# Optimization experiments

Measured on AMD Instinct MI355X. Metric: run time of the kernel, lower is better.

Reference implementation:

```python
import jax, jax.numpy as jnp
import numpy as np

N = 100000      # nodes
E = 1600000     # edges (avg degree 16)
F_IN, F_HID, F_OUT = 128, 64, 47


def setup_inputs() -> dict:
    key = jax.random.key(0)
    k1, k2, k3, k4 = jax.random.split(key, 4)
    x = jax.random.normal(k1, (N, F_IN), jnp.float32)
    edge_index = jax.random.randint(k2, (2, E), 0, N, jnp.int32)
    W1 = jax.random.normal(k3, (F_IN, F_HID), jnp.float32) * (1.0 / np.sqrt(F_IN))
    b1 = jnp.zeros((F_HID,), jnp.float32)
    W2 = jax.random.normal(k4, (F_HID, F_OUT), jnp.float32) * (1.0 / np.sqrt(F_HID))
    b2 = jnp.zeros((F_OUT,), jnp.float32)
    return {"x": x, "edge_index": edge_index, "W1": W1, "b1": b1, "W2": W2, "b2": b2}


def _gcn_conv(x, W, b, src, dst, n):
    """GCNConv with self-loops and symmetric normalization:
       out = D^{-1/2} (A + I) D^{-1/2} X W + b
    """
    xw = x @ W                                   # [N, F_out] transform first (small GEMM)
    # degree of A + I computed over destination nodes
    deg = jnp.ones((n,), xw.dtype).at[dst].add(1.0)      # [N]
    dinv = jax.lax.rsqrt(deg)                            # deg^{-1/2}
    norm = dinv[src] * dinv[dst]                         # [E]
    msg = xw[src] * norm[:, None]                        # [E, F_out] gather
    agg = jnp.zeros_like(xw).at[dst].add(msg)            # scatter-add aggregate
    agg = agg + xw * (1.0 / deg)[:, None]                # self-loop term: norm = 1/deg
    return agg + b


def reference(x, edge_index, W1, b1, W2, b2):
    src, dst = edge_index[0], edge_index[1]
    n = x.shape[0]
    h = _gcn_conv(x, W1, b1, src, dst, n)
    h = jax.nn.relu(h)
    # dropout is identity in eval mode (deterministic baseline)
    h = _gcn_conv(h, W2, b2, src, dst, n)
    return jax.nn.log_softmax(h, axis=1)
```

## Files before the change

### kernel.cpp

```cpp
#include <hip/hip_runtime.h>
#include <hip/hip_bf16.h>
#include <math.h>


#define CAP 48
#define NBSHIFT 8
#define SCNODES 256
#define BCAP 6144
typedef unsigned short u16;

__device__ __forceinline__ u16 f2bf(float f) {
    __hip_bfloat16 h = __float2bfloat16(f);
    return *reinterpret_cast<u16*>(&h);
}
__device__ __forceinline__ float bf2f(u16 u) {
    return __uint_as_float(((unsigned)u) << 16);
}


#define KC 32
#define KCP 36
#define GEMM_SMEM (64 * KCP * 4 + KC * 64 * 4)

__global__ __launch_bounds__(256) void gemm1_bin(const float* __restrict__ X,
                                                 const float* __restrict__ W,
                                                 u16* __restrict__ OUT,
                                                 const int* __restrict__ src,
                                                 const int* __restrict__ dst,
                                                 int* __restrict__ gtail,
                                                 int2* __restrict__ bucketed,
                                                 int N, int E, int NB, int seg, int GB) {
    __shared__ __align__(16) char smem[GEMM_SMEM];
    const int t = threadIdx.x;

    if ((int)blockIdx.x < GB) {
        float* xs = (float*)smem;
        float* Wp = (float*)(smem + 64 * KCP * 4);
        const int row0 = blockIdx.x * 64;
        const int c4 = (t & 15) * 4;
        const int r4 = (t >> 4) * 4;
        float acc[4][4] = {};

        for (int k0 = 0; k0 < 128; k0 += KC) {
            const float4* W4 = reinterpret_cast<const float4*>(W + k0 * 64);
            #pragma unroll
            for (int i = t; i < KC * 16; i += 256)
                reinterpret_cast<float4*>(Wp)[i] = W4[i];
            #pragma unroll
            for (int i = t; i < 64 * 8; i += 256) {
                int r = i >> 3, kq = i & 7;
                int m = row0 + r;
                float4 v = make_float4(0.f, 0.f, 0.f, 0.f);
                if (m < N) v = *reinterpret_cast<const float4*>(&X[(size_t)m * 128 + k0 + kq * 4]);
                *reinterpret_cast<float4*>(&xs[r * KCP + kq * 4]) = v;
            }
            __syncthreads();

            for (int k = 0; k < KC; k += 4) {
                float4 A[4], B[4];
                #pragma unroll
                for (int i = 0; i < 4; i++)
                    A[i] = *reinterpret_cast<const float4*>(&xs[(r4 + i) * KCP + k]);
                #pragma unroll
                for (int kk = 0; kk < 4; kk++)
                    B[kk] = *reinterpret_cast<const float4*>(&Wp[(k + kk) * 64 + c4]);
                const float* Af = reinterpret_cast<const float*>(A);
                const float* Bf = reinterpret_cast<const float*>(B);
                #pragma unroll
                for (int i = 0; i < 4; i++)
                    #pragma unroll
                    for (int kk = 0; kk < 4; kk++) {
                        float av = Af[i * 4 + kk];
                        #pragma unroll
                        for (int j = 0; j < 4; j++)
                            acc[i][j] = fmaf(av, Bf[kk * 4 + j], acc[i][j]);
                    }
            }
            __syncthreads();
        }
        #pragma unroll
        for (int i = 0; i < 4; i++) {
            int m = row0 + r4 + i;
            if (m >= N) continue;
            ushort4 o;
            o.x = f2bf(acc[i][0]); o.y = f2bf(acc[i][1]);
            o.z = f2bf(acc[i][2]); o.w = f2bf(acc[i][3]);
            *reinterpret_cast<ushort4*>(&OUT[(size_t)m * 64 + c4]) = o;
        }
    } else {
        int* hist = (int*)smem;
        int* base = hist + 512;
        const int bid = blockIdx.x - GB;

        const int b0 = bid * seg;
        const int b1 = min(b0 + seg, E);
        for (int i = t; i < NB; i += 256) hist[i] = 0;
        __syncthreads();
        for (int e = b0 + t; e < b1; e += 256)
            atomicAdd(&hist[dst[e] >> NBSHIFT], 1);
        __syncthreads();
        for (int i = t; i < NB; i += 256) {
            int h = hist[i];
            base[i] = h ? atomicAdd(&gtail[i], h) : 0;
            hist[i] = 0;
        }
        __syncthreads();
        for (int e = b0 + t; e < b1; e += 256) {
            int d = dst[e];
            int b = d >> NBSHIFT;
            int idx = base[b] + atomicAdd(&hist[b], 1);
            if (idx < BCAP) bucketed[(size_t)b * BCAP + idx] = make_int2(src[e], d);
        }
    }
}


__global__ __launch_bounds__(512) void scatter_csr(const int2* __restrict__ bucketed,
                                                   const int* __restrict__ gtail,
                                                   int* __restrict__ cnt,
                                                   int* __restrict__ csr_src,
                                                   float* __restrict__ dinv, int N) {
    __shared__ int cntL[SCNODES];
    __shared__ __align__(16) int csrL[SCNODES * CAP];
    const int b = blockIdx.x;
    const int t = threadIdx.x;
    for (int i = t; i < SCNODES; i += 512) cntL[i] = 0;
    __syncthreads();

    int n = gtail[b]; if (n > BCAP) n = BCAP;
    const int2* p = bucketed + (size_t)b * BCAP;
    for (int i = t; i < n; i += 512) {
        int2 e = p[i];
        int l = e.y & (SCNODES - 1);
        int slot = atomicAdd(&cntL[l], 1);
        if (slot < CAP) csrL[l * CAP + slot] = e.x;
    }
    __syncthreads();

    const int v0 = b << NBSHIFT;
    const int lim = min(SCNODES, N - v0);
    if (lim <= 0) return;
    int4* dst4 = reinterpret_cast<int4*>(&csr_src[(size_t)v0 * CAP]);
    const int4* src4 = reinterpret_cast<const int4*>(csrL);
    for (int i = t; i < lim * (CAP / 4); i += 512) dst4[i] = src4[i];
    for (int i = t; i < lim; i += 512) {
        int cv = cntL[i];
        cnt[v0 + i] = cv;
        dinv[v0 + i] = rsqrtf((float)cv + 1.0f);
    }
}


__global__ __launch_bounds__(256) void gemm2_tiled(const u16* __restrict__ X,
                                                   const float* __restrict__ W,
                                                   u16* __restrict__ OUT, int N) {
    __shared__ __align__(16) char smem[GEMM_SMEM];
    float* xs = (float*)smem;
    float* Wp = (float*)(smem + 64 * KCP * 4);
    const int t = threadIdx.x;
    const int row0 = blockIdx.x * 64;
    const int c4 = (t & 15) * 4;
    const int r4 = (t >> 4) * 4;
    float acc[4][4] = {};

    for (int k0 = 0; k0 < 64; k0 += KC) {
        for (int i = t; i < KC * 64; i += 256) {
            int k = i >> 6, c = i & 63;
            Wp[i] = (c < 47) ? W[(k0 + k) * 47 + c] : 0.f;
        }
        {
            int i = t;
            int r = i >> 2, kq = i & 3;
            int m = row0 + r;
            uint4 q = make_uint4(0u, 0u, 0u, 0u);
            if (m < N) q = *reinterpret_cast<const uint4*>(&X[(size_t)m * 64 + k0 + kq * 8]);
            float f0o = bf2f(q.x & 0xffffu), f1 = bf2f(q.x >> 16);
            float f2 = bf2f(q.y & 0xffffu), f3 = bf2f(q.y >> 16);
            float f4 = bf2f(q.z & 0xffffu), f5 = bf2f(q.z >> 16);
            float f6 = bf2f(q.w & 0xffffu), f7 = bf2f(q.w >> 16);
            float* dstp = &xs[r * KCP + kq * 8];
            *reinterpret_cast<float4*>(dstp)     = make_float4(f0o, f1, f2, f3);
            *reinterpret_cast<float4*>(dstp + 4) = make_float4(f4, f5, f6, f7);
        }
        __syncthreads();

        for (int k = 0; k < KC; k += 4) {
            float4 A[4], B[4];
            #pragma unroll
            for (int i = 0; i < 4; i++)
                A[i] = *reinterpret_cast<const float4*>(&xs[(r4 + i) * KCP + k]);
            #pragma unroll
            for (int kk = 0; kk < 4; kk++)
                B[kk] = *reinterpret_cast<const float4*>(&Wp[(k + kk) * 64 + c4]);
            const float* Af = reinterpret_cast<const float*>(A);
            const float* Bf = reinterpret_cast<const float*>(B);
            #pragma unroll
            for (int i = 0; i < 4; i++)
                #pragma unroll
                for (int kk = 0; kk < 4; kk++) {
                    float av = Af[i * 4 + kk];
                    #pragma unroll
                    for (int j = 0; j < 4; j++)
                        acc[i][j] = fmaf(av, Bf[kk * 4 + j], acc[i][j]);
                }
        }
        __syncthreads();
    }
    #pragma unroll
    for (int i = 0; i < 4; i++) {
        int m = row0 + r4 + i;
        if (m >= N) continue;
        ushort4 o;
        o.x = f2bf(acc[i][0]); o.y = f2bf(acc[i][1]);
        o.z = f2bf(acc[i][2]); o.w = f2bf(acc[i][3]);
        *reinterpret_cast<ushort4*>(&OUT[(size_t)m * 64 + c4]) = o;
    }
}

__device__ __forceinline__ void fma_bf8(uint4 q, float w, float* acc) {
    acc[0] = fmaf(__uint_as_float(q.x << 16),          w, acc[0]);
    acc[1] = fmaf(__uint_as_float(q.x & 0xffff0000u),  w, acc[1]);
    acc[2] = fmaf(__uint_as_float(q.y << 16),          w, acc[2]);
    acc[3] = fmaf(__uint_as_float(q.y & 0xffff0000u),  w, acc[3]);
    acc[4] = fmaf(__uint_as_float(q.z << 16),          w, acc[4]);
    acc[5] = fmaf(__uint_as_float(q.z & 0xffff0000u),  w, acc[5]);
    acc[6] = fmaf(__uint_as_float(q.w << 16),          w, acc[6]);
    acc[7] = fmaf(__uint_as_float(q.w & 0xffff0000u),  w, acc[7]);
}


__global__ __launch_bounds__(256, 4) void agg1_relu(const u16* __restrict__ xw,
                                                    const int* __restrict__ csr_src,
                                                    const int* __restrict__ cnt,
                                                    const float* __restrict__ dinv,
                                                    const float* __restrict__ bias,
                                                    u16* __restrict__ h, int N) {
    const int wid = (blockIdx.x * 256 + threadIdx.x) >> 6;
    const int lane = threadIdx.x & 63;
    const int v = wid * 2 + (lane >> 5);
    if (wid * 2 >= N) return;
    const bool okv = v < N;
    const int vs = okv ? v : 0;
    const int hl = lane & 31;
    int c = okv ? cnt[vs] : 0; if (c > CAP - 1) c = CAP - 1;
    const float dv = okv ? dinv[vs] : 0.f;
    int rawA = csr_src[vs * CAP + hl];
    int sA; float wA;
    if (hl < c)        { sA = rawA; wA = dinv[sA] * dv; }
    else if (hl == c)  { sA = vs;   wA = dv * dv; }
    else               { sA = 0;    wA = 0.f; }

    int ce = c + 1;
    int cemax = max(ce, __shfl_xor(ce, 32));
    const int r = hl >> 3, b = hl & 7;
    const int base = lane & 32;
    float acc[8] = {};

    {
        int s8[8]; float w8[8];
        #pragma unroll
        for (int u = 0; u < 8; u++) {
            int e = u * 4 + r;
            s8[u] = __shfl(sA, base + e);
            w8[u] = __shfl(wA, base + e);
        }
        uint4 q8[8];
        #pragma unroll
        for (int u = 0; u < 8; u++)
            if (u * 4 < cemax)
                q8[u] = *reinterpret_cast<const uint4*>(&xw[(size_t)s8[u] * 64 + b * 8]);
        #pragma unroll
        for (int u = 0; u < 8; u++)
            if (u * 4 < cemax) fma_bf8(q8[u], w8[u], acc);
    }
    if (cemax > 32) {
        int rawB = csr_src[vs * CAP + 32 + hl];
        int hl32 = hl + 32;
        int sB; float wB;
        if (hl32 < c)       { sB = rawB; wB = dinv[sB] * dv; }
        else if (hl32 == c) { sB = vs;   wB = dv * dv; }
        else                { sB = 0;    wB = 0.f; }
        int s8[8]; float w8[8];
        #pragma unroll
        for (int u = 0; u < 8; u++) {
            int e = u * 4 + r;
            s8[u] = __shfl(sB, base + e);
            w8[u] = __shfl(wB, base + e);
        }
        uint4 q8[8];
        #pragma unroll
        for (int u = 0; u < 8; u++)
            if (32 + u * 4 < cemax)
                q8[u] = *reinterpret_cast<const uint4*>(&xw[(size_t)s8[u] * 64 + b * 8]);
        #pragma unroll
        for (int u = 0; u < 8; u++)
            if (32 + u * 4 < cemax) fma_bf8(q8[u], w8[u], acc);
    }

    #pragma unroll
    for (int u = 0; u < 8; u++) {
        acc[u] += __shfl_xor(acc[u], 8);
        acc[u] += __shfl_xor(acc[u], 16);
    }
    if (r == 0 && okv) {
        ushort4 oA, oB;
        oA.x = f2bf(fmaxf(acc[0] + bias[b * 8 + 0], 0.f));
        oA.y = f2bf(fmaxf(acc[1] + bias[b * 8 + 1], 0.f));
        oA.z = f2bf(fmaxf(acc[2] + bias[b * 8 + 2], 0.f));
        oA.w = f2bf(fmaxf(acc[3] + bias[b * 8 + 3], 0.f));
        oB.x = f2bf(fmaxf(acc[4] + bias[b * 8 + 4], 0.f));
        oB.y = f2bf(fmaxf(acc[5] + bias[b * 8 + 5], 0.f));
        oB.z = f2bf(fmaxf(acc[6] + bias[b * 8 + 6], 0.f));
        oB.w = f2bf(fmaxf(acc[7] + bias[b * 8 + 7], 0.f));
        u16* dstp = &h[(size_t)v * 64 + b * 8];
        *reinterpret_cast<ushort4*>(dstp)     = oA;
        *reinterpret_cast<ushort4*>(dstp + 4) = oB;
    }
}


__global__ __launch_bounds__(256, 4) void agg2_lsm(const u16* __restrict__ hw,
                                                   const int* __restrict__ csr_src,
                                                   const int* __restrict__ cnt,
                                                   const float* __restrict__ dinv,
                                                   const float* __restrict__ bias,
                                                   float* __restrict__ out, int N) {
    const int wid = (blockIdx.x * 256 + threadIdx.x) >> 6;
    const int lane = threadIdx.x & 63;
    const int v = wid * 2 + (lane >> 5);
    if (wid * 2 >= N) return;
    const bool okv = v < N;
    const int vs = okv ? v : 0;
    const int hl = lane & 31;
    int c = okv ? cnt[vs] : 0; if (c > CAP - 1) c = CAP - 1;
    const float dv = okv ? dinv[vs] : 0.f;
    int rawA = csr_src[vs * CAP + hl];
    int sA; float wA;
    if (hl < c)        { sA = rawA; wA = dinv[sA] * dv; }
    else if (hl == c)  { sA = vs;   wA = dv * dv; }
    else               { sA = 0;    wA = 0.f; }

    int ce = c + 1;
    int cemax = max(ce, __shfl_xor(ce, 32));
    const int r = hl >> 3, b = hl & 7;
    const int base = lane & 32;
    float acc[8] = {};

    {
        int s8[8]; float w8[8];
        #pragma unroll
        for (int u = 0; u < 8; u++) {
            int e = u * 4 + r;
            s8[u] = __shfl(sA, base + e);
            w8[u] = __shfl(wA, base + e);
        }
        uint4 q8[8];
        #pragma unroll
        for (int u = 0; u < 8; u++)
            if (u * 4 < cemax)
                q8[u] = *reinterpret_cast<const uint4*>(&hw[(size_t)s8[u] * 64 + b * 8]);
        #pragma unroll
        for (int u = 0; u < 8; u++)
            if (u * 4 < cemax) fma_bf8(q8[u], w8[u], acc);
    }
    if (cemax > 32) {
        int rawB = csr_src[vs * CAP + 32 + hl];
        int hl32 = hl + 32;
        int sB; float wB;
        if (hl32 < c)       { sB = rawB; wB = dinv[sB] * dv; }
        else if (hl32 == c) { sB = vs;   wB = dv * dv; }
        else                { sB = 0;    wB = 0.f; }
        int s8[8]; float w8[8];
        #pragma unroll
        for (int u = 0; u < 8; u++) {
            int e = u * 4 + r;
            s8[u] = __shfl(sB, base + e);
            w8[u] = __shfl(wB, base + e);
        }
        uint4 q8[8];
        #pragma unroll
        for (int u = 0; u < 8; u++)
            if (32 + u * 4 < cemax)
                q8[u] = *reinterpret_cast<const uint4*>(&hw[(size_t)s8[u] * 64 + b * 8]);
        #pragma unroll
        for (int u = 0; u < 8; u++)
            if (32 + u * 4 < cemax) fma_bf8(q8[u], w8[u], acc);
    }

    #pragma unroll
    for (int u = 0; u < 8; u++) {
        acc[u] += __shfl_xor(acc[u], 8);
        acc[u] += __shfl_xor(acc[u], 16);
    }
    const int f0 = b * 8;
    float val[8];
    #pragma unroll
    for (int u = 0; u < 8; u++) {
        int f = f0 + u;
        val[u] = (f < 47) ? acc[u] + bias[f] : -INFINITY;
    }
    float m = val[0];
    #pragma unroll
    for (int u = 1; u < 8; u++) m = fmaxf(m, val[u]);
    m = fmaxf(m, __shfl_xor(m, 1));
    m = fmaxf(m, __shfl_xor(m, 2));
    m = fmaxf(m, __shfl_xor(m, 4));
    float s = 0.f;
    #pragma unroll
    for (int u = 0; u < 8; u++)
        s += (f0 + u < 47) ? __expf(val[u] - m) : 0.f;
    s += __shfl_xor(s, 1);
    s += __shfl_xor(s, 2);
    s += __shfl_xor(s, 4);
    float ls = m + __logf(s);
    if (r == 0 && okv) {
        #pragma unroll
        for (int u = 0; u < 8; u++) {
            int f = f0 + u;
            if (f < 47) out[(size_t)v * 47 + f] = val[u] - ls;
        }
    }
}


extern "C" void kernel_launch(void* const* d_in, const int* in_sizes, int n_in,
                              void* d_out, int out_size, void* d_ws, size_t ws_size,
                              hipStream_t stream) {
    const float* x  = (const float*)d_in[0];
    const int*   ei = (const int*)d_in[1];
    const float* W1 = (const float*)d_in[2];
    const float* b1 = (const float*)d_in[3];
    const float* W2 = (const float*)d_in[4];
    const float* b2 = (const float*)d_in[5];
    float* out = (float*)d_out;

    const int N = in_sizes[0] / 128;
    const int E = in_sizes[1] / 2;
    const int* src = ei;
    const int* dst = ei + E;
    const int NB = ((N - 1) >> NBSHIFT) + 1;

    char* ws = (char*)d_ws;
    size_t off = 0;
    auto alloc = [&](size_t bytes) {
        void* p = ws + off;
        off += (bytes + 255) & ~(size_t)255;
        return p;
    };
    int*   cnt      = (int*)  alloc((size_t)N * 4);
    int*   gtail    = (int*)  alloc((size_t)512 * 4);
    float* dinv     = (float*)alloc((size_t)N * 4);
    int*   csr_src  = (int*)  alloc(((size_t)N * CAP + 64) * 4);
    u16*   xw1      = (u16*)  alloc((size_t)N * 64 * 2);
    int2*  bucketed = (int2*) alloc((size_t)NB * BCAP * 8);
    u16*   hbuf     = (u16*)  alloc((size_t)N * 64 * 2);
    u16*   hw2      = (u16*)  alloc((size_t)N * 64 * 2);

    hipMemsetAsync(gtail, 0, 512 * 4, stream);

    const int GB = (N + 63) / 64;
    const int gridA = 512;
    const int seg = (E + gridA - 1) / gridA;
    gemm1_bin<<<GB + gridA, 256, 0, stream>>>(x, W1, xw1, src, dst, gtail, bucketed,
                                              N, E, NB, seg, GB);
    scatter_csr<<<NB, 512, 0, stream>>>(bucketed, gtail, cnt, csr_src, dinv, N);
    agg1_relu<<<(N + 7) / 8, 256, 0, stream>>>(xw1, csr_src, cnt, dinv, b1, hbuf, N);
    gemm2_tiled<<<(N + 63) / 64, 256, 0, stream>>>(hbuf, W2, hw2, N);
    agg2_lsm<<<(N + 7) / 8, 256, 0, stream>>>(hw2, csr_src, cnt, dinv, b2, out, N);
}
```

Baseline: 259.1 us.

## Load full K tile in gemm1 and stage bucketed edges in shared memory before writing

The first GEMM now loads the entire 64x128 X tile and all of W into shared memory at once, dropping the per-KC chunk loop and its barriers. The binning branch adds a block-local prefix scan over bucket counts and stages edge records sorted by bucket in shared memory. It then writes each bucket's records to global memory as contiguous runs, replacing the scattered per-edge writes. Shared memory per block grows to about 66KB, which may lower occupancy, and a segment larger than the staging buffer would overflow.

```diff
diff --git a/kernel.cpp b/kernel.cpp
--- a/kernel.cpp
+++ b/kernel.cpp
@@ -7,6 +7,7 @@
 #define NBSHIFT 8
 #define SCNODES 256
 #define BCAP 6144
+#define SEGMAX 3200
 typedef unsigned short u16;
 
 __device__ __forceinline__ u16 f2bf(float f) {
@@ -18,9 +19,8 @@
 }
 
 
-#define KC 32
-#define KCP 36
-#define GEMM_SMEM (64 * KCP * 4 + KC * 64 * 4)
+#define XSTRIDE 132
+#define GEMM_SMEM (64 * XSTRIDE * 4 + 128 * 64 * 4)
 
 __global__ __launch_bounds__(256) void gemm1_bin(const float* __restrict__ X,
                                                  const float* __restrict__ W,
@@ -35,48 +35,48 @@
 
     if ((int)blockIdx.x < GB) {
         float* xs = (float*)smem;
-        float* Wp = (float*)(smem + 64 * KCP * 4);
+        float* Wp = (float*)(smem + 64 * XSTRIDE * 4);
         const int row0 = blockIdx.x * 64;
         const int c4 = (t & 15) * 4;
         const int r4 = (t >> 4) * 4;
         float acc[4][4] = {};
 
-        for (int k0 = 0; k0 < 128; k0 += KC) {
-            const float4* W4 = reinterpret_cast<const float4*>(W + k0 * 64);
-            #pragma unroll
-            for (int i = t; i < KC * 16; i += 256)
-                reinterpret_cast<float4*>(Wp)[i] = W4[i];
-            #pragma unroll
-            for (int i = t; i < 64 * 8; i += 256) {
-                int r = i >> 3, kq = i & 7;
-                int m = row0 + r;
-                float4 v = make_float4(0.f, 0.f, 0.f, 0.f);
-                if (m < N) v = *reinterpret_cast<const float4*>(&X[(size_t)m * 128 + k0 + kq * 4]);
-                *reinterpret_cast<float4*>(&xs[r * KCP + kq * 4]) = v;
-            }
-            __syncthreads();
-
-            for (int k = 0; k < KC; k += 4) {
-                float4 A[4], B[4];
+        #pragma unroll
+        for (int i = t; i < 64 * 32; i += 256) {
+            int r = i >> 5, kq = i & 31;
+            int m = row0 + r;
+            float4 v = make_float4(0.f, 0.f, 0.f, 0.f);
+            if (m < N) v = *reinterpret_cast<const float4*>(&X[(size_t)m * 128 + kq * 4]);
+            *reinterpret_cast<float4*>(&xs[r * XSTRIDE + kq * 4]) = v;
+        }
+        {
+            const float4* W4 = reinterpret_cast<const float4*>(W);
+            float4* Wp4 = reinterpret_cast<float4*>(Wp);
+            #pragma unroll
+            for (int i = t; i < 128 * 16; i += 256) Wp4[i] = W4[i];
+        }
+        __syncthreads();
+
+        #pragma unroll 2
+        for (int k = 0; k < 128; k += 4) {
+            float4 A[4], B[4];
+            #pragma unroll
+            for (int i = 0; i < 4; i++)
+                A[i] = *reinterpret_cast<const float4*>(&xs[(r4 + i) * XSTRIDE + k]);
+            #pragma unroll
+            for (int kk = 0; kk < 4; kk++)
+                B[kk] = *reinterpret_cast<const float4*>(&Wp[(k + kk) * 64 + c4]);
+            const float* Af = reinterpret_cast<const float*>(A);
+            const float* Bf = reinterpret_cast<const float*>(B);
+            #pragma unroll
+            for (int i = 0; i < 4; i++)
                 #pragma unroll
-                for (int i = 0; i < 4; i++)
-                    A[i] = *reinterpret_cast<const float4*>(&xs[(r4 + i) * KCP + k]);
-                #pragma unroll
-                for (int kk = 0; kk < 4; kk++)
-                    B[kk] = *reinterpret_cast<const float4*>(&Wp[(k + kk) * 64 + c4]);
-                const float* Af = reinterpret_cast<const float*>(A);
-                const float* Bf = reinterpret_cast<const float*>(B);
-                #pragma unroll
-                for (int i = 0; i < 4; i++)
+                for (int kk = 0; kk < 4; kk++) {
+                    float av = Af[i * 4 + kk];
                     #pragma unroll
-                    for (int kk = 0; kk < 4; kk++) {
-                        float av = Af[i * 4 + kk];
-                        #pragma unroll
-                        for (int j = 0; j < 4; j++)
-                            acc[i][j] = fmaf(av, Bf[kk * 4 + j], acc[i][j]);
-                    }
-            }
-            __syncthreads();
+                    for (int j = 0; j < 4; j++)
+                        acc[i][j] = fmaf(av, Bf[kk * 4 + j], acc[i][j]);
+                }
         }
         #pragma unroll
         for (int i = 0; i < 4; i++) {
@@ -88,28 +88,49 @@
             *reinterpret_cast<ushort4*>(&OUT[(size_t)m * 64 + c4]) = o;
         }
     } else {
-        int* hist = (int*)smem;
-        int* base = hist + 512;
+        int*  hist = (int*)smem;
+        int*  scan = hist + 512;
+        int*  gbase = scan + 512;
+        int2* srec = (int2*)(smem + 6144);
         const int bid = blockIdx.x - GB;
 
         const int b0 = bid * seg;
         const int b1 = min(b0 + seg, E);
-        for (int i = t; i < NB; i += 256) hist[i] = 0;
+        const int n = b1 - b0;
+
+        hist[t] = 0; hist[t + 256] = 0;
         __syncthreads();
         for (int e = b0 + t; e < b1; e += 256)
             atomicAdd(&hist[dst[e] >> NBSHIFT], 1);
         __syncthreads();
-        for (int i = t; i < NB; i += 256) {
-            int h = hist[i];
-            base[i] = h ? atomicAdd(&gtail[i], h) : 0;
-            hist[i] = 0;
-        }
+        int c0 = hist[t], c1 = hist[t + 256];
+        gbase[t]       = c0 ? atomicAdd(&gtail[t], c0) : 0;
+        gbase[t + 256] = c1 ? atomicAdd(&gtail[t + 256], c1) : 0;
+        scan[t] = c0; scan[t + 256] = c1;
+        hist[t] = 0; hist[t + 256] = 0;
+        __syncthreads();
+        #pragma unroll
+        for (int d = 1; d < 512; d <<= 1) {
+            int v0 = (t >= d) ? scan[t - d] : 0;
+            int v1 = scan[t + 256 - d];
+            __syncthreads();
+            scan[t] += v0; scan[t + 256] += v1;
+            __syncthreads();
+        }
+        scan[t] -= c0; scan[t + 256] -= c1;
         __syncthreads();
         for (int e = b0 + t; e < b1; e += 256) {
             int d = dst[e];
             int b = d >> NBSHIFT;
-            int idx = base[b] + atomicAdd(&hist[b], 1);
-            if (idx < BCAP) bucketed[(size_t)b * BCAP + idx] = make_int2(src[e], d);
+            int off = atomicAdd(&hist[b], 1);
+            srec[scan[b] + off] = make_int2(src[e], d);
+        }
+        __syncthreads();
+        for (int i = t; i < n; i += 256) {
+            int2 rec = srec[i];
+            int b = rec.y >> NBSHIFT;
+            int gpos = gbase[b] + (i - scan[b]);
+            if (gpos < BCAP) bucketed[(size_t)b * BCAP + gpos] = rec;
         }
     }
 }
@@ -151,10 +172,14 @@
 }
 
 
+#define KC 32
+#define KCP 36
+#define G2_SMEM (64 * KCP * 4 + KC * 64 * 4)
+
 __global__ __launch_bounds__(256) void gemm2_tiled(const u16* __restrict__ X,
                                                    const float* __restrict__ W,
                                                    u16* __restrict__ OUT, int N) {
-    __shared__ __align__(16) char smem[GEMM_SMEM];
+    __shared__ __align__(16) char smem[G2_SMEM];
     float* xs = (float*)smem;
     float* Wp = (float*)(smem + 64 * KCP * 4);
     const int t = threadIdx.x;
```

After: 261.0 us. Within noise of the previous version (+0.7%).

## Stage binned edges in shared memory and pack records to 32-bit

Applied to the files above, without the earlier changes.

Binning blocks now compute a local prefix scan over the per-bucket counts and first stage each edge record in shared memory grouped by bucket. Each thread then copies a whole bucket's contiguous run to global memory, which replaces scattered 8-byte stores. Each record is packed into one int (src shifted left by 8, OR'd with the local node index), halving bucket traffic for both the write and the scatter_csr read. The binning blocks are reordered to launch before the GEMM blocks, and shared memory grows to hold the staging area. The trade-offs are that the copy-out is a serial per-thread loop with uneven bucket sizes, the packing assumes src fits in 24 bits, and there is leftover dead code.

```diff
diff --git a/kernel.cpp b/kernel.cpp
--- a/kernel.cpp
+++ b/kernel.cpp
@@ -7,6 +7,7 @@
 #define NBSHIFT 8
 #define SCNODES 256
 #define BCAP 6144
+#define SEGMAX 3200
 typedef unsigned short u16;
 
 __device__ __forceinline__ u16 f2bf(float f) {
@@ -20,7 +21,7 @@
 
 #define KC 32
 #define KCP 36
-#define GEMM_SMEM (64 * KCP * 4 + KC * 64 * 4)
+#define FUSED_SMEM 18944
 
 __global__ __launch_bounds__(256) void gemm1_bin(const float* __restrict__ X,
                                                  const float* __restrict__ W,
@@ -28,15 +29,15 @@
                                                  const int* __restrict__ src,
                                                  const int* __restrict__ dst,
                                                  int* __restrict__ gtail,
-                                                 int2* __restrict__ bucketed,
-                                                 int N, int E, int NB, int seg, int GB) {
-    __shared__ __align__(16) char smem[GEMM_SMEM];
+                                                 int* __restrict__ bucketed,
+                                                 int N, int E, int NB, int seg, int BINB) {
+    __shared__ __align__(16) char smem[FUSED_SMEM];
     const int t = threadIdx.x;
 
-    if ((int)blockIdx.x < GB) {
+    if ((int)blockIdx.x >= BINB) {
         float* xs = (float*)smem;
         float* Wp = (float*)(smem + 64 * KCP * 4);
-        const int row0 = blockIdx.x * 64;
+        const int row0 = (blockIdx.x - BINB) * 64;
         const int c4 = (t & 15) * 4;
         const int r4 = (t >> 4) * 4;
         float acc[4][4] = {};
@@ -88,34 +89,68 @@
             *reinterpret_cast<ushort4*>(&OUT[(size_t)m * 64 + c4]) = o;
         }
     } else {
-        int* hist = (int*)smem;
-        int* base = hist + 512;
-        const int bid = blockIdx.x - GB;
+        int* hist  = (int*)smem;
+        int* scan  = hist + 512;
+        int* gbase = scan + 512;
+        int* srec  = (int*)(smem + 6144);
+        const int bid = blockIdx.x;
 
         const int b0 = bid * seg;
         const int b1 = min(b0 + seg, E);
-        for (int i = t; i < NB; i += 256) hist[i] = 0;
+        const int n = b1 - b0;
+
+        hist[t] = 0; hist[t + 256] = 0;
         __syncthreads();
         for (int e = b0 + t; e < b1; e += 256)
             atomicAdd(&hist[dst[e] >> NBSHIFT], 1);
         __syncthreads();
-        for (int i = t; i < NB; i += 256) {
-            int h = hist[i];
-            base[i] = h ? atomicAdd(&gtail[i], h) : 0;
-            hist[i] = 0;
-        }
+        int c0 = hist[t], c1 = hist[t + 256];
+        gbase[t]       = c0 ? atomicAdd(&gtail[t], c0) : 0;
+        gbase[t + 256] = c1 ? atomicAdd(&gtail[t + 256], c1) : 0;
+        scan[t] = c0; scan[t + 256] = c1;
+        hist[t] = 0; hist[t + 256] = 0;
+        __syncthreads();
+        #pragma unroll
+        for (int d = 1; d < 512; d <<= 1) {
+            int v0 = (t >= d) ? scan[t - d] : 0;
+            int v1 = scan[t + 256 - d];
+            __syncthreads();
+            scan[t] += v0; scan[t + 256] += v1;
+            __syncthreads();
+        }
+        scan[t] -= c0; scan[t + 256] -= c1;
         __syncthreads();
         for (int e = b0 + t; e < b1; e += 256) {
             int d = dst[e];
             int b = d >> NBSHIFT;
-            int idx = base[b] + atomicAdd(&hist[b], 1);
-            if (idx < BCAP) bucketed[(size_t)b * BCAP + idx] = make_int2(src[e], d);
-        }
-    }
-}
-
-
-__global__ __launch_bounds__(512) void scatter_csr(const int2* __restrict__ bucketed,
+            int off = atomicAdd(&hist[b], 1);
+            srec[scan[b] + off] = (src[e] << NBSHIFT) | (d & (SCNODES - 1));
+        }
+        __syncthreads();
+        for (int i = t; i < n; i += 256) {
+            int rec = srec[i];
+            (void)rec;
+            break;
+        }
+        for (int b = t; b < 512; b += 256) {
+            int cnt_b = (b < 256) ? c0 : c1;
+            (void)cnt_b;
+        }
+        __syncthreads();
+        for (int b = t; b < NB; b += 256) {
+            int lb = scan[b];
+            int le = (b + 1 < 512) ? scan[b + 1] : n;
+            int gb = gbase[b];
+            for (int i = lb; i < le; i++) {
+                int gpos = gb + (i - lb);
+                if (gpos < BCAP) bucketed[(size_t)b * BCAP + gpos] = srec[i];
+            }
+        }
+    }
+}
+
+
+__global__ __launch_bounds__(512) void scatter_csr(const int* __restrict__ bucketed,
                                                    const int* __restrict__ gtail,
                                                    int* __restrict__ cnt,
                                                    int* __restrict__ csr_src,
@@ -128,12 +163,12 @@
     __syncthreads();
 
     int n = gtail[b]; if (n > BCAP) n = BCAP;
-    const int2* p = bucketed + (size_t)b * BCAP;
+    const int* p = bucketed + (size_t)b * BCAP;
     for (int i = t; i < n; i += 512) {
-        int2 e = p[i];
-        int l = e.y & (SCNODES - 1);
+        int rec = p[i];
+        int l = rec & (SCNODES - 1);
         int slot = atomicAdd(&cntL[l], 1);
-        if (slot < CAP) csrL[l * CAP + slot] = e.x;
+        if (slot < CAP) csrL[l * CAP + slot] = rec >> NBSHIFT;
     }
     __syncthreads();
 
@@ -151,10 +186,12 @@
 }
 
 
+#define G2_SMEM (64 * KCP * 4 + KC * 64 * 4)
+
 __global__ __launch_bounds__(256) void gemm2_tiled(const u16* __restrict__ X,
                                                    const float* __restrict__ W,
                                                    u16* __restrict__ OUT, int N) {
-    __shared__ __align__(16) char smem[GEMM_SMEM];
+    __shared__ __align__(16) char smem[G2_SMEM];
     float* xs = (float*)smem;
     float* Wp = (float*)(smem + 64 * KCP * 4);
     const int t = threadIdx.x;
@@ -452,17 +489,17 @@
     float* dinv     = (float*)alloc((size_t)N * 4);
     int*   csr_src  = (int*)  alloc(((size_t)N * CAP + 64) * 4);
     u16*   xw1      = (u16*)  alloc((size_t)N * 64 * 2);
-    int2*  bucketed = (int2*) alloc((size_t)NB * BCAP * 8);
+    int*   bucketed = (int*)  alloc((size_t)NB * BCAP * 4);
     u16*   hbuf     = (u16*)  alloc((size_t)N * 64 * 2);
     u16*   hw2      = (u16*)  alloc((size_t)N * 64 * 2);
 
     hipMemsetAsync(gtail, 0, 512 * 4, stream);
 
     const int GB = (N + 63) / 64;
-    const int gridA = 512;
-    const int seg = (E + gridA - 1) / gridA;
-    gemm1_bin<<<GB + gridA, 256, 0, stream>>>(x, W1, xw1, src, dst, gtail, bucketed,
-                                              N, E, NB, seg, GB);
+    const int BINB = 512;
+    const int seg = (E + BINB - 1) / BINB;
+    gemm1_bin<<<BINB + GB, 256, 0, stream>>>(x, W1, xw1, src, dst, gtail, bucketed,
+                                             N, E, NB, seg, BINB);
     scatter_csr<<<NB, 512, 0, stream>>>(bucketed, gtail, cnt, csr_src, dinv, N);
     agg1_relu<<<(N + 7) / 8, 256, 0, stream>>>(xw1, csr_src, cnt, dinv, b1, hbuf, N);
     gemm2_tiled<<<(N + 63) / 64, 256, 0, stream>>>(hbuf, W2, hw2, N);
```

After: 253.2 us. 1.02x faster.
